# Performance work log

Hardware: AMD Instinct MI355X
Metric: run time of the kernel (lower is better)

Reference implementation:

```python
import jax, jax.numpy as jnp
import numpy as np

BATCH = 8192
DIM = 256
TEMP = 0.001
EPS = 1e-12  # torch F.normalize eps


def setup_inputs() -> dict:
    key = jax.random.key(0)
    k1, k2 = jax.random.split(key)
    proj_1 = jax.random.normal(k1, (BATCH, DIM), dtype=jnp.float32)
    proj_2 = jax.random.normal(k2, (BATCH, DIM), dtype=jnp.float32)
    return {"proj_1": proj_1, "proj_2": proj_2}


def _l2_normalize(x):
    norm = jnp.maximum(jnp.linalg.norm(x, axis=1, keepdims=True), EPS)
    return x / norm


def reference(proj_1, proj_2):
    # L2-normalize rows (SimCLR z_i, z_j)
    z_i = _l2_normalize(proj_1)  # [B, D]
    z_j = _l2_normalize(proj_2)  # [B, D]
    # cosine similarity of unit vectors == dot product -> single matmul
    sim = jnp.einsum("id,jd->ij", z_i, z_j)  # [B, B]
    positives = jnp.diagonal(sim)  # [B]
    n = positives / TEMP
    all_losses = -n + jax.scipy.special.logsumexp(sim / TEMP, axis=1)
    loss = jnp.sum(all_losses) / BATCH
    return (loss, jnp.sum(positives))
```

## Files before the change

kernel.cpp:

```cpp
#include <hip/hip_runtime.h>
#include <hip/hip_fp8.h>
#include <stdint.h>
#include <stddef.h>

#define BATCH 8192
#define DIM   256

#define LN2F 0.6931471805599453f
#define SCALE_ZJ 16.0f
#define SCALE_ZI 90.16844005556021f

typedef int   v8i    __attribute__((ext_vector_type(8)));
typedef float f32x16 __attribute__((ext_vector_type(16)));


static __device__ __forceinline__ uint8_t f2fp8(float f) {
  __hip_fp8_e4m3 q(f);
  return *reinterpret_cast<uint8_t*>(&q);
}

__global__ __launch_bounds__(256) void prep_kernel(
    const float* __restrict__ p1, const float* __restrict__ p2,
    uint8_t* __restrict__ Zi8, uint8_t* __restrict__ Zj8,
    float* __restrict__ pos) {
  const int lane = threadIdx.x & 63;
  const int w    = threadIdx.x >> 6;
  const int row  = blockIdx.x * 4 + w;

  const float4 x1 = ((const float4*)p1)[row * 64 + lane];
  const float4 x2 = ((const float4*)p2)[row * 64 + lane];
  float ss1 = x1.x * x1.x + x1.y * x1.y + x1.z * x1.z + x1.w * x1.w;
  float ss2 = x2.x * x2.x + x2.y * x2.y + x2.z * x2.z + x2.w * x2.w;
  float d   = x1.x * x2.x + x1.y * x2.y + x1.z * x2.z + x1.w * x2.w;
#pragma unroll
  for (int m = 1; m < 64; m <<= 1) {
    ss1 += __shfl_xor(ss1, m);
    ss2 += __shfl_xor(ss2, m);
    d   += __shfl_xor(d, m);
  }
  const float n1 = fmaxf(sqrtf(ss1), 1e-12f);
  const float n2 = fmaxf(sqrtf(ss2), 1e-12f);
  if (lane == 0) pos[row] = d / (n1 * n2);

  const float sI = SCALE_ZI / n1;
  const float sJ = SCALE_ZJ / n2;
  uchar4 u1, u2;
  u1.x = f2fp8(x1.x * sI); u1.y = f2fp8(x1.y * sI);
  u1.z = f2fp8(x1.z * sI); u1.w = f2fp8(x1.w * sI);
  u2.x = f2fp8(x2.x * sJ); u2.y = f2fp8(x2.y * sJ);
  u2.z = f2fp8(x2.z * sJ); u2.w = f2fp8(x2.w * sJ);

  const size_t tb = (size_t)(row >> 5) * 8192;
  const int off = (lane >> 4) * 2048 + ((lane >> 2) & 1) * 1024 +
                  (((lane >> 3) & 1) * 32 + (row & 31)) * 16 + (lane & 3) * 4;
  *(uchar4*)(Zi8 + tb + off) = u1;
  *(uchar4*)(Zj8 + tb + off) = u2;
}

static __device__ __forceinline__ void lse_update(const f32x16& acc,
                                                  float& m, float& l) {
  float t0 = fmaxf(fmaxf(acc[0],  acc[1]),  acc[2]);
  float t1 = fmaxf(fmaxf(acc[3],  acc[4]),  acc[5]);
  float t2 = fmaxf(fmaxf(acc[6],  acc[7]),  acc[8]);
  float t3 = fmaxf(fmaxf(acc[9],  acc[10]), acc[11]);
  t0 = fmaxf(fmaxf(t0, t1), fmaxf(fmaxf(acc[12], acc[13]), acc[14]));
  t2 = fmaxf(fmaxf(t2, t3), acc[15]);
  const float mn = fmaxf(m, fmaxf(t0, t2));
  float s0 = 0.f, s1 = 0.f;
#pragma unroll
  for (int r = 0; r < 16; r += 2) {
    s0 += __builtin_amdgcn_exp2f(acc[r + 0] - mn);
    s1 += __builtin_amdgcn_exp2f(acc[r + 1] - mn);
  }
  l = l * __builtin_amdgcn_exp2f(m - mn) + (s0 + s1);
  m = mn;
}

__global__ __launch_bounds__(256, 3) void lse_kernel(
    const uint8_t* __restrict__ Zi8, const uint8_t* __restrict__ Zj8,
    float* __restrict__ plse) {
  const int bid   = blockIdx.x;
  const int chunk = bid & 63;
  const int rb    = bid >> 6;
  const int tid   = threadIdx.x;
  const int lane  = tid & 63;
  const int r32   = lane & 31;
  const int h     = lane >> 5;
  const int w     = tid >> 6;
  const int iBase = rb * 256 + w * 64;

  __shared__ __align__(16) uint8_t lds[32768];

  const uint8_t* src = Zj8 + (size_t)chunk * 32768;
#pragma unroll
  for (int it = 0; it < 8; ++it) {
    const int off = it * 4096 + tid * 16;
    __builtin_amdgcn_global_load_lds(
        (const __attribute__((address_space(1))) void*)(src + off),
        (__attribute__((address_space(3))) void*)(lds + off), 16, 0, 0);
  }

  v8i b0[4], b1[4];
  const uint8_t* zb = Zi8 + (size_t)(rb * 8 + w * 2) * 8192 + lane * 16;
#pragma unroll
  for (int q = 0; q < 4; ++q) {
    union { int4 i4[2]; v8i v; } u0, u1;
    u0.i4[0] = *(const int4*)(zb + q * 2048);
    u0.i4[1] = *(const int4*)(zb + q * 2048 + 1024);
    u1.i4[0] = *(const int4*)(zb + 8192 + q * 2048);
    u1.i4[1] = *(const int4*)(zb + 8192 + q * 2048 + 1024);
    b0[q] = u0.v; b1[q] = u1.v;
  }
#pragma unroll
  for (int q = 0; q < 4; ++q) { asm("" : "+v"(b0[q])); asm("" : "+v"(b1[q])); }

  float m0 = -1e30f, l0 = 0.f, m1 = -1e30f, l1 = 0.f;

  __syncthreads();

#pragma unroll
  for (int t = 0; t < 4; ++t) {
    const uint8_t* buf = lds + t * 8192 + lane * 16;
    f32x16 acc0 = {}, acc1 = {};
#pragma unroll
    for (int q = 0; q < 4; ++q) {
      union { int4 i4[2]; v8i v; } ua;
      ua.i4[0] = *(const int4*)(buf + q * 2048);
      ua.i4[1] = *(const int4*)(buf + q * 2048 + 1024);
      acc0 = __builtin_amdgcn_mfma_scale_f32_32x32x64_f8f6f4(
          ua.v, b0[q], acc0, 0, 0, 0, 0x7F7F7F7F, 0, 0x7F7F7F7F);
      acc1 = __builtin_amdgcn_mfma_scale_f32_32x32x64_f8f6f4(
          ua.v, b1[q], acc1, 0, 0, 0, 0x7F7F7F7F, 0, 0x7F7F7F7F);
    }
    lse_update(acc0, m0, l0);
    lse_update(acc1, m1, l1);
  }

#pragma unroll
  for (int p = 0; p < 2; ++p) {
    float m = p ? m1 : m0;
    float l = p ? l1 : l0;
    const float mo = __shfl_xor(m, 32);
    const float lo = __shfl_xor(l, 32);
    const float mn = fmaxf(m, mo);
    l = l * __builtin_amdgcn_exp2f(m - mn) + lo * __builtin_amdgcn_exp2f(mo - mn);
    if (h == 0) {
      const int i = iBase + p * 32 + r32;
      plse[(size_t)chunk * BATCH + i] = mn + __builtin_amdgcn_logf(l);
    }
  }
}

__global__ __launch_bounds__(256) void finalize_kernel(
    const float* __restrict__ plse, const float* __restrict__ pos,
    float2* __restrict__ bpart, unsigned int* __restrict__ counter,
    float* __restrict__ out) {
  const int tid = threadIdx.x;
  const int row = blockIdx.x * 256 + tid;
  float v[64];
#pragma unroll
  for (int c = 0; c < 64; ++c) v[c] = plse[(size_t)c * BATCH + row];
  float M = v[0];
#pragma unroll
  for (int c = 1; c < 64; ++c) M = fmaxf(M, v[c]);
  float S = 0.0f;
#pragma unroll
  for (int c = 0; c < 64; ++c) S += __builtin_amdgcn_exp2f(v[c] - M);
  const float lse = LN2F * (M + __builtin_amdgcn_logf(S));
  const float pv  = pos[row];
  float lsum = lse - 1000.0f * pv;
  float psum = pv;
#pragma unroll
  for (int msk = 1; msk < 64; msk <<= 1) {
    lsum += __shfl_xor(lsum, msk);
    psum += __shfl_xor(psum, msk);
  }
  __shared__ float sl[4], sp[4];
  const int w = tid >> 6, lane = tid & 63;
  if (lane == 0) { sl[w] = lsum; sp[w] = psum; }
  __syncthreads();
  if (tid == 0) {
    union { float2 f; unsigned long long u; } pk;
    pk.f = make_float2(sl[0] + sl[1] + sl[2] + sl[3],
                       sp[0] + sp[1] + sp[2] + sp[3]);
    __hip_atomic_store((unsigned long long*)&bpart[blockIdx.x], pk.u,
                       __ATOMIC_RELEASE, __HIP_MEMORY_SCOPE_AGENT);
    const unsigned int t = __hip_atomic_fetch_add(
        counter, 1u, __ATOMIC_ACQ_REL, __HIP_MEMORY_SCOPE_AGENT);
    if (t == 31u) {
      float L = 0.f, P = 0.f;
#pragma unroll
      for (int i = 0; i < 32; ++i) {
        union { float2 f; unsigned long long u; } q2;
        q2.u = __hip_atomic_load((const unsigned long long*)&bpart[i],
                                 __ATOMIC_ACQUIRE, __HIP_MEMORY_SCOPE_AGENT);
        L += q2.f.x; P += q2.f.y;
      }
      out[0] = L / (float)BATCH;
      out[1] = P;
    }
  }
}

extern "C" void kernel_launch(void* const* d_in, const int* in_sizes, int n_in,
                              void* d_out, int out_size, void* d_ws, size_t ws_size,
                              hipStream_t stream) {
  const float* p1 = (const float*)d_in[0];
  const float* p2 = (const float*)d_in[1];
  float* out = (float*)d_out;
  uint8_t* ws = (uint8_t*)d_ws;

  uint8_t* Zi8          = ws;
  uint8_t* Zj8          = ws + (size_t)2 * 1024 * 1024;
  float* pos            = (float*)(ws + (size_t)4 * 1024 * 1024);
  float2* bpart         = (float2*)(ws + (size_t)4 * 1024 * 1024 + 32 * 1024);
  unsigned int* counter = (unsigned int*)(ws + (size_t)4 * 1024 * 1024 + 40 * 1024);
  float* plse           = (float*)(ws + (size_t)4 * 1024 * 1024 + 64 * 1024);

  hipMemsetAsync(counter, 0, sizeof(unsigned int), stream);
  prep_kernel<<<dim3(2048), dim3(256), 0, stream>>>(p1, p2, Zi8, Zj8, pos);
  lse_kernel<<<dim3(2048), dim3(256), 0, stream>>>(Zi8, Zj8, plse);
  finalize_kernel<<<dim3(32), dim3(256), 0, stream>>>(plse, pos, bpart, counter, out);
}
```

Measured before the change: 46.11 us.

## Switch LSE tile to 16x16x128 FP8 MFMA with matching layout and row-major partials

Swaps the 32x32x64 scaled FP8 MFMA for the 16x16x128 variant. The prep kernel's packed layout and the LSE kernel's load, accumulate and reduce paths change to match, and the per-row reduction now uses a two-step cross-lane shuffle. Occupancy hint rises from 3 to 4 blocks and s_setprio is placed around the MFMA bursts. Partial LSEs are stored row-major so the finalize kernel can read them with float4 loads. The aim is to cut accumulator register pressure, raise occupancy and improve finalize memory access, at the cost of more MFMA issues and more reduction shuffles.

Result: slower. 146.7 us (+218.1%).

```diff
diff --git a/kernel.cpp b/kernel.cpp
--- a/kernel.cpp
+++ b/kernel.cpp
@@ -10,13 +10,18 @@
 #define SCALE_ZJ 16.0f
 #define SCALE_ZI 90.16844005556021f
 
-typedef int   v8i    __attribute__((ext_vector_type(8)));
-typedef float f32x16 __attribute__((ext_vector_type(16)));
+typedef int   v4i   __attribute__((ext_vector_type(4)));
+typedef int   v8i   __attribute__((ext_vector_type(8)));
+typedef float f32x4 __attribute__((ext_vector_type(4)));
 
 
 static __device__ __forceinline__ uint8_t f2fp8(float f) {
   __hip_fp8_e4m3 q(f);
   return *reinterpret_cast<uint8_t*>(&q);
+}
+
+static __device__ __forceinline__ v8i cat8(v4i lo, v4i hi) {
+  return __builtin_shufflevector(lo, hi, 0, 1, 2, 3, 4, 5, 6, 7);
 }
 
 __global__ __launch_bounds__(256) void prep_kernel(
@@ -50,33 +55,26 @@
   u2.x = f2fp8(x2.x * sJ); u2.y = f2fp8(x2.y * sJ);
   u2.z = f2fp8(x2.z * sJ); u2.w = f2fp8(x2.w * sJ);
 
-  const size_t tb = (size_t)(row >> 5) * 8192;
-  const int off = (lane >> 4) * 2048 + ((lane >> 2) & 1) * 1024 +
-                  (((lane >> 3) & 1) * 32 + (row & 31)) * 16 + (lane & 3) * 4;
+  const size_t tb = (size_t)(row >> 4) * 4096;
+  const int off = (lane >> 5) * 2048 + ((lane >> 2) & 1) * 1024 +
+                  (((lane >> 3) & 3) * 16 + (row & 15)) * 16 + (lane & 3) * 4;
   *(uchar4*)(Zi8 + tb + off) = u1;
   *(uchar4*)(Zj8 + tb + off) = u2;
 }
 
-static __device__ __forceinline__ void lse_update(const f32x16& acc,
-                                                  float& m, float& l) {
-  float t0 = fmaxf(fmaxf(acc[0],  acc[1]),  acc[2]);
-  float t1 = fmaxf(fmaxf(acc[3],  acc[4]),  acc[5]);
-  float t2 = fmaxf(fmaxf(acc[6],  acc[7]),  acc[8]);
-  float t3 = fmaxf(fmaxf(acc[9],  acc[10]), acc[11]);
-  t0 = fmaxf(fmaxf(t0, t1), fmaxf(fmaxf(acc[12], acc[13]), acc[14]));
-  t2 = fmaxf(fmaxf(t2, t3), acc[15]);
-  const float mn = fmaxf(m, fmaxf(t0, t2));
-  float s0 = 0.f, s1 = 0.f;
-#pragma unroll
-  for (int r = 0; r < 16; r += 2) {
-    s0 += __builtin_amdgcn_exp2f(acc[r + 0] - mn);
-    s1 += __builtin_amdgcn_exp2f(acc[r + 1] - mn);
-  }
-  l = l * __builtin_amdgcn_exp2f(m - mn) + (s0 + s1);
+static __device__ __forceinline__ void lse_update4(const f32x4& a,
+                                                   float& m, float& l) {
+  const float tmax = fmaxf(fmaxf(a[0], a[1]), fmaxf(a[2], a[3]));
+  const float mn = fmaxf(m, tmax);
+  const float sum = (__builtin_amdgcn_exp2f(a[0] - mn) +
+                     __builtin_amdgcn_exp2f(a[1] - mn)) +
+                    (__builtin_amdgcn_exp2f(a[2] - mn) +
+                     __builtin_amdgcn_exp2f(a[3] - mn));
+  l = l * __builtin_amdgcn_exp2f(m - mn) + sum;
   m = mn;
 }
 
-__global__ __launch_bounds__(256, 3) void lse_kernel(
+__global__ __launch_bounds__(256, 4) void lse_kernel(
     const uint8_t* __restrict__ Zi8, const uint8_t* __restrict__ Zj8,
     float* __restrict__ plse) {
   const int bid   = blockIdx.x;
@@ -84,8 +82,7 @@
   const int rb    = bid >> 6;
   const int tid   = threadIdx.x;
   const int lane  = tid & 63;
-  const int r32   = lane & 31;
-  const int h     = lane >> 5;
+  const int r16   = lane & 15;
   const int w     = tid >> 6;
   const int iBase = rb * 256 + w * 64;
 
@@ -100,53 +97,68 @@
         (__attribute__((address_space(3))) void*)(lds + off), 16, 0, 0);
   }
 
-  v8i b0[4], b1[4];
-  const uint8_t* zb = Zi8 + (size_t)(rb * 8 + w * 2) * 8192 + lane * 16;
-#pragma unroll
-  for (int q = 0; q < 4; ++q) {
-    union { int4 i4[2]; v8i v; } u0, u1;
-    u0.i4[0] = *(const int4*)(zb + q * 2048);
-    u0.i4[1] = *(const int4*)(zb + q * 2048 + 1024);
-    u1.i4[0] = *(const int4*)(zb + 8192 + q * 2048);
-    u1.i4[1] = *(const int4*)(zb + 8192 + q * 2048 + 1024);
-    b0[q] = u0.v; b1[q] = u1.v;
-  }
-#pragma unroll
-  for (int q = 0; q < 4; ++q) { asm("" : "+v"(b0[q])); asm("" : "+v"(b1[q])); }
-
-  float m0 = -1e30f, l0 = 0.f, m1 = -1e30f, l1 = 0.f;
+  v8i b[4][2];
+  const uint8_t* zb = Zi8 + (size_t)(rb * 16 + w * 4) * 4096 + lane * 16;
+#pragma unroll
+  for (int it = 0; it < 4; ++it) {
+#pragma unroll
+    for (int s = 0; s < 2; ++s) {
+      const uint8_t* base = zb + it * 4096 + s * 2048;
+      b[it][s] = cat8(*(const v4i*)(base), *(const v4i*)(base + 1024));
+    }
+  }
+#pragma unroll
+  for (int it = 0; it < 4; ++it) {
+    asm("" : "+v"(b[it][0]));
+    asm("" : "+v"(b[it][1]));
+  }
+
+  float m[4], l[4];
+#pragma unroll
+  for (int it = 0; it < 4; ++it) { m[it] = -1e30f; l[it] = 0.f; }
 
   __syncthreads();
 
 #pragma unroll
-  for (int t = 0; t < 4; ++t) {
-    const uint8_t* buf = lds + t * 8192 + lane * 16;
-    f32x16 acc0 = {}, acc1 = {};
-#pragma unroll
-    for (int q = 0; q < 4; ++q) {
-      union { int4 i4[2]; v8i v; } ua;
-      ua.i4[0] = *(const int4*)(buf + q * 2048);
-      ua.i4[1] = *(const int4*)(buf + q * 2048 + 1024);
-      acc0 = __builtin_amdgcn_mfma_scale_f32_32x32x64_f8f6f4(
-          ua.v, b0[q], acc0, 0, 0, 0, 0x7F7F7F7F, 0, 0x7F7F7F7F);
-      acc1 = __builtin_amdgcn_mfma_scale_f32_32x32x64_f8f6f4(
-          ua.v, b1[q], acc1, 0, 0, 0, 0x7F7F7F7F, 0, 0x7F7F7F7F);
-    }
-    lse_update(acc0, m0, l0);
-    lse_update(acc1, m1, l1);
-  }
-
-#pragma unroll
-  for (int p = 0; p < 2; ++p) {
-    float m = p ? m1 : m0;
-    float l = p ? l1 : l0;
-    const float mo = __shfl_xor(m, 32);
-    const float lo = __shfl_xor(l, 32);
-    const float mn = fmaxf(m, mo);
-    l = l * __builtin_amdgcn_exp2f(m - mn) + lo * __builtin_amdgcn_exp2f(mo - mn);
-    if (h == 0) {
-      const int i = iBase + p * 32 + r32;
-      plse[(size_t)chunk * BATCH + i] = mn + __builtin_amdgcn_logf(l);
+  for (int t = 0; t < 8; ++t) {
+    const uint8_t* buf = lds + t * 4096 + lane * 16;
+    f32x4 acc0 = {}, acc1 = {}, acc2 = {}, acc3 = {};
+    __builtin_amdgcn_s_setprio(1);
+#pragma unroll
+    for (int s = 0; s < 2; ++s) {
+      const v8i av = cat8(*(const v4i*)(buf + s * 2048),
+                          *(const v4i*)(buf + s * 2048 + 1024));
+      acc0 = __builtin_amdgcn_mfma_scale_f32_16x16x128_f8f6f4(
+          av, b[0][s], acc0, 0, 0, 0, 0x7F7F7F7F, 0, 0x7F7F7F7F);
+      acc1 = __builtin_amdgcn_mfma_scale_f32_16x16x128_f8f6f4(
+          av, b[1][s], acc1, 0, 0, 0, 0x7F7F7F7F, 0, 0x7F7F7F7F);
+      acc2 = __builtin_amdgcn_mfma_scale_f32_16x16x128_f8f6f4(
+          av, b[2][s], acc2, 0, 0, 0, 0x7F7F7F7F, 0, 0x7F7F7F7F);
+      acc3 = __builtin_amdgcn_mfma_scale_f32_16x16x128_f8f6f4(
+          av, b[3][s], acc3, 0, 0, 0, 0x7F7F7F7F, 0, 0x7F7F7F7F);
+    }
+    __builtin_amdgcn_s_setprio(0);
+    lse_update4(acc0, m[0], l[0]);
+    lse_update4(acc1, m[1], l[1]);
+    lse_update4(acc2, m[2], l[2]);
+    lse_update4(acc3, m[3], l[3]);
+  }
+
+#pragma unroll
+  for (int it = 0; it < 4; ++it) {
+    float mm = m[it], ll = l[it];
+#pragma unroll
+    for (int msk = 16; msk < 64; msk <<= 1) {
+      const float mo = __shfl_xor(mm, msk);
+      const float lo = __shfl_xor(ll, msk);
+      const float mn = fmaxf(mm, mo);
+      ll = ll * __builtin_amdgcn_exp2f(mm - mn) +
+           lo * __builtin_amdgcn_exp2f(mo - mn);
+      mm = mn;
+    }
+    if (lane < 16) {
+      const int i = iBase + it * 16 + r16;
+      plse[(size_t)i * 64 + chunk] = mm + __builtin_amdgcn_logf(ll);
     }
   }
 }
@@ -159,7 +171,10 @@
   const int row = blockIdx.x * 256 + tid;
   float v[64];
 #pragma unroll
-  for (int c = 0; c < 64; ++c) v[c] = plse[(size_t)c * BATCH + row];
+  for (int c = 0; c < 16; ++c) {
+    const float4 q = ((const float4*)(plse + (size_t)row * 64))[c];
+    v[c * 4 + 0] = q.x; v[c * 4 + 1] = q.y; v[c * 4 + 2] = q.z; v[c * 4 + 3] = q.w;
+  }
   float M = v[0];
 #pragma unroll
   for (int c = 1; c < 64; ++c) M = fmaxf(M, v[c]);
```
